# Optimization experiments

Measured on AMD Instinct MI355X. Metric: run time of the kernel, lower is better.

## Reference

```python
import jax, jax.numpy as jnp
import numpy as np
import math

D_MODEL = 1024
N_HEAD = 16
D_K = D_MODEL // N_HEAD
NEG_INF = -1e30  # fp32 mask fill value used by the torch module


def _rope(x, b_rotate=None):
    # x: [b, h, n, k], k even. Interleaved (even/odd) RoPE, matching the torch code.
    b, h, n, k = x.shape
    half = k // 2
    inv_freq = 1.0 / (10000.0 ** (jnp.arange(half, dtype=jnp.float32) / half))  # [half]
    ang = jnp.arange(n, dtype=jnp.float32)[:, None] * inv_freq[None, :]          # [n, half]
    sin = jnp.sin(ang)
    cos = jnp.cos(ang)
    x1 = x[..., 0::2]  # [b,h,n,half]
    x2 = x[..., 1::2]
    even = x1 * cos - x2 * sin
    odd = x1 * sin + x2 * cos
    out = jnp.stack([even, odd], axis=-1).reshape(b, h, n, k)  # re-interleave
    if b_rotate is not None:
        out = out * b_rotate  # barope multiplicative term
    return out


def setup_inputs() -> dict:
    key = jax.random.key(0)
    ks = jax.random.split(key, 7)
    B, S = 1, 2048
    query = jax.random.normal(ks[0], (B, S, D_MODEL), dtype=jnp.float32)
    kk = jax.random.normal(ks[1], (B, S, D_MODEL), dtype=jnp.float32)
    value = jax.random.normal(ks[2], (B, S, D_MODEL), dtype=jnp.float32)
    b_emb = jax.random.normal(ks[3], (B, S, D_MODEL), dtype=jnp.float32)
    mask = jax.random.bernoulli(ks[4], 0.9, (B, S))  # bool [B,S]
    linear_layers = 0.02 * jax.random.normal(ks[5], (3, D_MODEL, N_HEAD, D_K), dtype=jnp.float32)
    b_proj = jax.random.normal(ks[6], (D_MODEL, N_HEAD, D_K), dtype=jnp.float32)
    return {"query": query, "key": kk, "value": value, "b_emb": b_emb,
            "mask": mask, "linear_layers": linear_layers, "b_proj": b_proj}


def reference(query, key, value, b_emb, mask, linear_layers, b_proj):
    B, S, _ = query.shape
    # QKV projections: [b,n,d] x [d,h,k] -> [b,h,n,k]
    q = jnp.einsum('bnd,dhk->bhnk', query, linear_layers[0])
    k = jnp.einsum('bnd,dhk->bhnk', key, linear_layers[1])
    v = jnp.einsum('bnd,dhk->bhnk', value, linear_layers[2])
    # barope=True branch: multiplicative rotation modifier from b_emb
    b_rotate = jnp.einsum('bnd,dhk->bhnk', b_emb, b_proj)
    q = _rope(q, b_rotate)
    k = _rope(k, b_rotate)
    scores = jnp.einsum('bhqk,bhmk->bhqm', q, k) / math.sqrt(D_K)  # [b,h,s,s]
    pair_mask = (mask[:, :, None] & mask[:, None, :])[:, None]     # [b,1,s,s]
    scores = jnp.where(pair_mask, scores, NEG_INF)
    p_attn = jax.nn.softmax(scores, axis=-1)  # dropout p=0 -> identity
    x = jnp.einsum('bhqm,bhmk->bhqk', p_attn, v)
    return x.transpose(0, 2, 1, 3).reshape(B, S, N_HEAD * D_K)
```

## Files before the change

### kernel.cpp

```cpp
#include <hip/hip_runtime.h>
#include <hip/hip_bf16.h>
#include <math.h>

#define S_LEN 2048
#define NHEAD 16
#define DMODEL 1024

typedef short bf16x8 __attribute__((ext_vector_type(8)));
typedef float f32x4 __attribute__((ext_vector_type(4)));

static __device__ __forceinline__ unsigned short bfbits(float x) {
    __hip_bfloat16 h = __float2bfloat16(x);
    unsigned short u; __builtin_memcpy(&u, &h, 2); return u;
}
static __device__ __forceinline__ float bf2f(unsigned short u) {
    union { unsigned int i; float f; } v; v.i = ((unsigned int)u) << 16; return v.f;
}
static __device__ __forceinline__ void splitRN(float x, unsigned short& hi, unsigned short& lo) {
    unsigned short h = bfbits(x);
    float r = x - bf2f(h);
    hi = h; lo = bfbits(r);
}
static __device__ __forceinline__ void split4(float4 x, ushort4& h4, ushort4& l4) {
    unsigned short h0,l0,h1,l1,h2,l2,h3,l3;
    splitRN(x.x,h0,l0); splitRN(x.y,h1,l1); splitRN(x.z,h2,l2); splitRN(x.w,h3,l3);
    h4 = make_ushort4(h0,h1,h2,h3); l4 = make_ushort4(l0,l1,l2,l3);
}

__device__ __forceinline__ int mask_at(const void* mp, int enc, int s) {
    if (enc) return ((const unsigned char*)mp)[s] != 0;
    return ((const unsigned int*)mp)[s] != 0u;
}

__global__ void detect_kernel(const void* __restrict__ mask, int* __restrict__ flags) {
    if (threadIdx.x == 0 && blockIdx.x == 0) {
        const unsigned int* m = (const unsigned int*)mask;
        int bytey = 0;
        for (int i = 0; i < 8; ++i) {
            unsigned int u = m[i];
            if (u != 0u && u != 1u && u != 0x3F800000u) bytey = 1;
        }
        flags[0] = bytey;
    }
}

__global__ __launch_bounds__(256)
void presplit_w(const float* __restrict__ ll, const float* __restrict__ bproj,
                unsigned short* __restrict__ Wh, unsigned short* __restrict__ Wl) {
    __shared__ unsigned short Th[64][72], Tl[64][72];
    const int t = threadIdx.x;
    const int bid = blockIdx.x;
    const int stream = bid >> 8;
    const int rem = bid & 255;
    const int h = rem >> 4;
    const int d0 = (rem & 15) << 6;
    const float* src = (stream == 3) ? bproj : (ll + (size_t)stream * 1048576);
#pragma unroll
    for (int rep = 0; rep < 4; ++rep) {
        int fid = rep * 256 + t;
        int dl = fid >> 4, n4 = (fid & 15) * 4;
        float4 w = *(const float4*)&src[(size_t)(d0 + dl) * 1024 + h * 64 + n4];
        unsigned short hh, lo2;
#pragma unroll
        for (int m = 0; m < 4; ++m) { splitRN((&w.x)[m], hh, lo2); Th[n4+m][dl] = hh; Tl[n4+m][dl] = lo2; }
    }
    __syncthreads();
    size_t obase = (size_t)stream * 1048576;
#pragma unroll
    for (int rep = 0; rep < 2; ++rep) {
        int wid = rep * 256 + t;
        int n = wid >> 3, dl8 = (wid & 7) * 8;
        int dtile = n >> 4, cc = n & 15;
        int dglob = d0 + dl8;
        int kc = dglob >> 5;
        int qd = (dglob >> 3) & 3;
        size_t off = obase + (size_t)(h * 4 + dtile) * 16384 + (size_t)kc * 512
                   + (size_t)(qd * 16 + cc) * 8;
        *(uint4*)&Wh[off] = *(uint4*)&Th[n][dl8];
        *(uint4*)&Wl[off] = *(uint4*)&Tl[n][dl8];
    }
}

__global__ __launch_bounds__(256, 2)
void proj_fused4(const float* __restrict__ Xq, const float* __restrict__ Xk,
                 const float* __restrict__ Xv, const float* __restrict__ Xb,
                 const unsigned short* __restrict__ Wh, const unsigned short* __restrict__ Wl,
                 unsigned short* __restrict__ qhi, unsigned short* __restrict__ qlo,
                 unsigned short* __restrict__ khi, unsigned short* __restrict__ klo,
                 unsigned short* __restrict__ vhi) {
    __shared__ unsigned short smem[17920];
    unsigned short (*XQh)[40] = (unsigned short(*)[40])(smem + 0 * 2560);
    unsigned short (*XQl)[40] = (unsigned short(*)[40])(smem + 1 * 2560);
    unsigned short (*XKh)[40] = (unsigned short(*)[40])(smem + 2 * 2560);
    unsigned short (*XKl)[40] = (unsigned short(*)[40])(smem + 3 * 2560);
    unsigned short (*XVh)[40] = (unsigned short(*)[40])(smem + 4 * 2560);
    unsigned short (*XBh)[40] = (unsigned short(*)[40])(smem + 5 * 2560);
    unsigned short (*XBl)[40] = (unsigned short(*)[40])(smem + 6 * 2560);
    unsigned short (*T0)[72] = (unsigned short(*)[72])(smem + 0 * 4608);
    unsigned short (*T1)[72] = (unsigned short(*)[72])(smem + 1 * 4608);
    unsigned short (*T2)[72] = (unsigned short(*)[72])(smem + 2 * 4608);

    const int t = threadIdx.x;
    const int lin = blockIdx.x + (blockIdx.y << 4);
    const int xcd = lin & 7;
    const int h = (lin >> 3) & 15;
    const int s0 = (xcd * 4 + (lin >> 7)) * 64;
    const int lane = t & 63, dt = t >> 6, quad = lane >> 4, c = lane & 15;

    f32x4 aq[4], ak[4], av[4], ab[4];
#pragma unroll
    for (int i = 0; i < 4; ++i) {
        aq[i] = (f32x4){0.f,0.f,0.f,0.f}; ak[i] = (f32x4){0.f,0.f,0.f,0.f};
        av[i] = (f32x4){0.f,0.f,0.f,0.f}; ab[i] = (f32x4){0.f,0.f,0.f,0.f};
    }

    const int xr = t >> 2, xk = (t & 3) * 8;
    const size_t xg = (size_t)(s0 + xr) * DMODEL + xk;
    const size_t wb = (size_t)(h * 4 + dt) * 16384 + (size_t)lane * 8;

    float4 pq[2], pk[2], pv[2], pb[2];
    pq[0] = *(const float4*)&Xq[xg]; pq[1] = *(const float4*)&Xq[xg + 4];
    pk[0] = *(const float4*)&Xk[xg]; pk[1] = *(const float4*)&Xk[xg + 4];
    pv[0] = *(const float4*)&Xv[xg]; pv[1] = *(const float4*)&Xv[xg + 4];
    pb[0] = *(const float4*)&Xb[xg]; pb[1] = *(const float4*)&Xb[xg + 4];

    bf16x8 wQh = *(const bf16x8*)&Wh[wb];
    bf16x8 wQl = *(const bf16x8*)&Wl[wb];
    bf16x8 wKh = *(const bf16x8*)&Wh[1048576 + wb];
    bf16x8 wKl = *(const bf16x8*)&Wl[1048576 + wb];
    bf16x8 wVh = *(const bf16x8*)&Wh[2097152 + wb];
    bf16x8 wVl = *(const bf16x8*)&Wl[2097152 + wb];
    bf16x8 wBh = *(const bf16x8*)&Wh[3145728 + wb];
    bf16x8 wBl = *(const bf16x8*)&Wl[3145728 + wb];

    for (int kc = 0; kc < 32; ++kc) {
        __syncthreads();
        {
            ushort4 h4, l4;
            split4(pq[0], h4, l4); *(ushort4*)&XQh[xr][xk]   = h4; *(ushort4*)&XQl[xr][xk]   = l4;
            split4(pq[1], h4, l4); *(ushort4*)&XQh[xr][xk+4] = h4; *(ushort4*)&XQl[xr][xk+4] = l4;
            split4(pk[0], h4, l4); *(ushort4*)&XKh[xr][xk]   = h4; *(ushort4*)&XKl[xr][xk]   = l4;
            split4(pk[1], h4, l4); *(ushort4*)&XKh[xr][xk+4] = h4; *(ushort4*)&XKl[xr][xk+4] = l4;
            split4(pb[0], h4, l4); *(ushort4*)&XBh[xr][xk]   = h4; *(ushort4*)&XBl[xr][xk]   = l4;
            split4(pb[1], h4, l4); *(ushort4*)&XBh[xr][xk+4] = h4; *(ushort4*)&XBl[xr][xk+4] = l4;
            *(ushort4*)&XVh[xr][xk]   = make_ushort4(bfbits(pv[0].x),bfbits(pv[0].y),bfbits(pv[0].z),bfbits(pv[0].w));
            *(ushort4*)&XVh[xr][xk+4] = make_ushort4(bfbits(pv[1].x),bfbits(pv[1].y),bfbits(pv[1].z),bfbits(pv[1].w));
        }
        __syncthreads();

        bf16x8 aQh = wQh, aQl = wQl, aKh = wKh, aKl = wKl;
        bf16x8 aVh = wVh, aVl = wVl, aBh = wBh, aBl = wBl;

        if (kc + 1 < 32) {
            size_t wo = wb + (size_t)(kc + 1) * 512;
            wQh = *(const bf16x8*)&Wh[wo];           wQl = *(const bf16x8*)&Wl[wo];
            wKh = *(const bf16x8*)&Wh[1048576 + wo]; wKl = *(const bf16x8*)&Wl[1048576 + wo];
            wVh = *(const bf16x8*)&Wh[2097152 + wo]; wVl = *(const bf16x8*)&Wl[2097152 + wo];
            wBh = *(const bf16x8*)&Wh[3145728 + wo]; wBl = *(const bf16x8*)&Wl[3145728 + wo];
            size_t g = xg + (size_t)(kc + 1) * 32;
            pq[0] = *(const float4*)&Xq[g]; pq[1] = *(const float4*)&Xq[g + 4];
            pk[0] = *(const float4*)&Xk[g]; pk[1] = *(const float4*)&Xk[g + 4];
            pv[0] = *(const float4*)&Xv[g]; pv[1] = *(const float4*)&Xv[g + 4];
            pb[0] = *(const float4*)&Xb[g]; pb[1] = *(const float4*)&Xb[g + 4];
        }

#pragma unroll
        for (int st = 0; st < 4; ++st) {
            bf16x8 b1 = *(bf16x8*)&XQh[st*16+c][quad*8];
            bf16x8 b2 = *(bf16x8*)&XQl[st*16+c][quad*8];
            aq[st] = __builtin_amdgcn_mfma_f32_16x16x32_bf16(aQh, b1, aq[st], 0, 0, 0);
            aq[st] = __builtin_amdgcn_mfma_f32_16x16x32_bf16(aQh, b2, aq[st], 0, 0, 0);
            aq[st] = __builtin_amdgcn_mfma_f32_16x16x32_bf16(aQl, b1, aq[st], 0, 0, 0);
            aq[st] = __builtin_amdgcn_mfma_f32_16x16x32_bf16(aQl, b2, aq[st], 0, 0, 0);
            b1 = *(bf16x8*)&XKh[st*16+c][quad*8];
            b2 = *(bf16x8*)&XKl[st*16+c][quad*8];
            ak[st] = __builtin_amdgcn_mfma_f32_16x16x32_bf16(aKh, b1, ak[st], 0, 0, 0);
            ak[st] = __builtin_amdgcn_mfma_f32_16x16x32_bf16(aKh, b2, ak[st], 0, 0, 0);
            ak[st] = __builtin_amdgcn_mfma_f32_16x16x32_bf16(aKl, b1, ak[st], 0, 0, 0);
            ak[st] = __builtin_amdgcn_mfma_f32_16x16x32_bf16(aKl, b2, ak[st], 0, 0, 0);
            b1 = *(bf16x8*)&XVh[st*16+c][quad*8];
            av[st] = __builtin_amdgcn_mfma_f32_16x16x32_bf16(aVh, b1, av[st], 0, 0, 0);
            av[st] = __builtin_amdgcn_mfma_f32_16x16x32_bf16(aVl, b1, av[st], 0, 0, 0);
            b1 = *(bf16x8*)&XBh[st*16+c][quad*8];
            b2 = *(bf16x8*)&XBl[st*16+c][quad*8];
            ab[st] = __builtin_amdgcn_mfma_f32_16x16x32_bf16(aBh, b1, ab[st], 0, 0, 0);
            ab[st] = __builtin_amdgcn_mfma_f32_16x16x32_bf16(aBh, b2, ab[st], 0, 0, 0);
            ab[st] = __builtin_amdgcn_mfma_f32_16x16x32_bf16(aBl, b1, ab[st], 0, 0, 0);
            ab[st] = __builtin_amdgcn_mfma_f32_16x16x32_bf16(aBl, b2, ab[st], 0, 0, 0);
        }
    }

    float rq[4][4], rk[4][4];
    {
        int p0 = dt * 8 + 2 * quad;
        double inv0 = pow(10000.0, -(double)p0 / 32.0);
        double inv1 = pow(10000.0, -(double)(p0 + 1) / 32.0);
#pragma unroll
        for (int st = 0; st < 4; ++st) {
            int s = s0 + st * 16 + c;
            double a0 = (double)s * inv0, a1 = (double)s * inv1;
            float sn0 = (float)sin(a0), cs0 = (float)cos(a0);
            float sn1 = (float)sin(a1), cs1 = (float)cos(a1);
            rq[st][0] = (aq[st][0]*cs0 - aq[st][1]*sn0) * ab[st][0];
            rq[st][1] = (aq[st][0]*sn0 + aq[st][1]*cs0) * ab[st][1];
            rq[st][2] = (aq[st][2]*cs1 - aq[st][3]*sn1) * ab[st][2];
            rq[st][3] = (aq[st][2]*sn1 + aq[st][3]*cs1) * ab[st][3];
            rk[st][0] = (ak[st][0]*cs0 - ak[st][1]*sn0) * ab[st][0];
            rk[st][1] = (ak[st][0]*sn0 + ak[st][1]*cs0) * ab[st][1];
            rk[st][2] = (ak[st][2]*cs1 - ak[st][3]*sn1) * ab[st][2];
            rk[st][3] = (ak[st][2]*sn1 + ak[st][3]*cs1) * ab[st][3];
        }
    }
    __syncthreads();
#pragma unroll
    for (int st = 0; st < 4; ++st) {
        unsigned short h0,l0,h1,l1,h2,l2,h3,l3;
        splitRN(rq[st][0],h0,l0); splitRN(rq[st][1],h1,l1);
        splitRN(rq[st][2],h2,l2); splitRN(rq[st][3],h3,l3);
        *(ushort4*)&T0[st*16+c][dt*16+4*quad] = make_ushort4(h0,h1,h2,h3);
        *(ushort4*)&T1[st*16+c][dt*16+4*quad] = make_ushort4(l0,l1,l2,l3);
#pragma unroll
        for (int reg = 0; reg < 4; ++reg)
            T2[dt * 16 + 4 * quad + reg][st * 16 + c] = bfbits(av[st][reg]);
    }
    __syncthreads();
#pragma unroll
    for (int i = 0; i < 2; ++i) {
        int id = i * 256 + t, row = id >> 3, d8 = (id & 7) * 8;
        size_t qb = ((size_t)(h * S_LEN + s0 + row)) * 64 + d8;
        *(uint4*)&qhi[qb] = *(uint4*)&T0[row][d8];
        *(uint4*)&qlo[qb] = *(uint4*)&T1[row][d8];
        size_t vb = ((size_t)(h * 64 + row)) * S_LEN + s0 + d8;
        *(uint4*)&vhi[vb] = *(uint4*)&T2[row][d8];
    }
    __syncthreads();
#pragma unroll
    for (int st = 0; st < 4; ++st) {
        unsigned short h0,l0,h1,l1,h2,l2,h3,l3;
        splitRN(rk[st][0],h0,l0); splitRN(rk[st][1],h1,l1);
        splitRN(rk[st][2],h2,l2); splitRN(rk[st][3],h3,l3);
        *(ushort4*)&T0[st*16+c][dt*16+4*quad] = make_ushort4(h0,h1,h2,h3);
        *(ushort4*)&T1[st*16+c][dt*16+4*quad] = make_ushort4(l0,l1,l2,l3);
    }
    __syncthreads();
#pragma unroll
    for (int i = 0; i < 2; ++i) {
        int id = i * 256 + t, row = id >> 3, d8 = (id & 7) * 8;
        size_t qb = ((size_t)(h * S_LEN + s0 + row)) * 64 + d8;
        *(uint4*)&khi[qb] = *(uint4*)&T0[row][d8];
        *(uint4*)&klo[qb] = *(uint4*)&T1[row][d8];
    }
}

__global__ __launch_bounds__(256)
void attn_mfma(const unsigned short* __restrict__ qh, const unsigned short* __restrict__ ql,
               const unsigned short* __restrict__ kh, const unsigned short* __restrict__ kl,
               const unsigned short* __restrict__ vh,
               const void* __restrict__ mask, float* __restrict__ out,
               const int* __restrict__ flags) {
    __shared__ unsigned short Kh[2][64][72], Kl[2][64][72];
    __shared__ unsigned short Vt[2][64][72];
    __shared__ unsigned short Sh[64][72], Sl[64][72];
    const int menc = flags[0];
    const int t = threadIdx.x;
    const int lin = blockIdx.x + (blockIdx.y << 5);
    const int h = (lin & 7) * 2 + ((lin >> 3) & 1);
    const int s0 = (lin >> 4) * 64;
    const int lane = t & 63, w = t >> 6, quad = lane >> 4, c = lane & 15;

    bf16x8 qfh[2], qfl[2];
#pragma unroll
    for (int ks = 0; ks < 2; ++ks) {
        size_t base = ((size_t)(h * S_LEN + s0 + 16 * w + c)) * 64 + ks * 32 + quad * 8;
        qfh[ks] = *(const bf16x8*)&qh[base];
        qfl[ks] = *(const bf16x8*)&ql[base];
    }
    int mq[4];
#pragma unroll
    for (int i = 0; i < 4; ++i) mq[i] = mask_at(mask, menc, s0 + 16 * w + quad * 4 + i);

    float m_i[4], l_i[4];
#pragma unroll
    for (int i = 0; i < 4; ++i) { m_i[i] = -INFINITY; l_i[i] = 0.0f; }
    f32x4 o_acc[4];
#pragma unroll
    for (int i = 0; i < 4; ++i) o_acc[i] = (f32x4){0.f,0.f,0.f,0.f};

    uint4 pre[6];
#pragma unroll
    for (int i = 0; i < 2; ++i) {
        int id = i * 256 + t, row = id >> 3, col8 = (id & 7) * 8;
        size_t kb = ((size_t)(h * S_LEN + row)) * 64 + col8;
        size_t vb = ((size_t)(h * 64 + row)) * S_LEN + col8;
        pre[0 + i] = *(const uint4*)&kh[kb];
        pre[2 + i] = *(const uint4*)&kl[kb];
        pre[4 + i] = *(const uint4*)&vh[vb];
    }
#pragma unroll
    for (int i = 0; i < 2; ++i) {
        int id = i * 256 + t, row = id >> 3, col8 = (id & 7) * 8;
        *(uint4*)&Kh[0][row][col8] = pre[0 + i];
        *(uint4*)&Kl[0][row][col8] = pre[2 + i];
        *(uint4*)&Vt[0][row][col8] = pre[4 + i];
    }
    __syncthreads();

    int cur = 0;
    for (int kt = 0; kt < 32; ++kt) {
        if (kt + 1 < 32) {
            const int kb0 = (kt + 1) * 64;
#pragma unroll
            for (int i = 0; i < 2; ++i) {
                int id = i * 256 + t, row = id >> 3, col8 = (id & 7) * 8;
                size_t kb = ((size_t)(h * S_LEN + kb0 + row)) * 64 + col8;
                size_t vb = ((size_t)(h * 64 + row)) * S_LEN + kb0 + col8;
                pre[0 + i] = *(const uint4*)&kh[kb];
                pre[2 + i] = *(const uint4*)&kl[kb];
                pre[4 + i] = *(const uint4*)&vh[vb];
            }
        }
        int mk[4];
#pragma unroll
        for (int nt = 0; nt < 4; ++nt) mk[nt] = mask_at(mask, menc, kt * 64 + 16 * nt + c);

        f32x4 sc[4];
#pragma unroll
        for (int i = 0; i < 4; ++i) sc[i] = (f32x4){0.f,0.f,0.f,0.f};
#pragma unroll
        for (int nt = 0; nt < 4; ++nt)
#pragma unroll
            for (int ks = 0; ks < 2; ++ks) {
                bf16x8 kfh = *(bf16x8*)&Kh[cur][nt * 16 + c][ks * 32 + quad * 8];
                bf16x8 kfl = *(bf16x8*)&Kl[cur][nt * 16 + c][ks * 32 + quad * 8];
                sc[nt] = __builtin_amdgcn_mfma_f32_16x16x32_bf16(qfh[ks], kfh, sc[nt], 0, 0, 0);
                sc[nt] = __builtin_amdgcn_mfma_f32_16x16x32_bf16(qfh[ks], kfl, sc[nt], 0, 0, 0);
                sc[nt] = __builtin_amdgcn_mfma_f32_16x16x32_bf16(qfl[ks], kfh, sc[nt], 0, 0, 0);
            }

        float sm[4][4];
#pragma unroll
        for (int nt = 0; nt < 4; ++nt)
#pragma unroll
            for (int reg = 0; reg < 4; ++reg)
                sm[nt][reg] = (mq[reg] && mk[nt]) ? sc[nt][reg] * 0.125f : -1e30f;

        float rmax[4];
#pragma unroll
        for (int reg = 0; reg < 4; ++reg)
            rmax[reg] = fmaxf(fmaxf(sm[0][reg], sm[1][reg]), fmaxf(sm[2][reg], sm[3][reg]));
#pragma unroll
        for (int off = 1; off <= 8; off <<= 1)
#pragma unroll
            for (int reg = 0; reg < 4; ++reg)
                rmax[reg] = fmaxf(rmax[reg], __shfl_xor(rmax[reg], off, 64));

        float mn[4], alpha[4];
#pragma unroll
        for (int reg = 0; reg < 4; ++reg) {
            mn[reg] = fmaxf(m_i[reg], rmax[reg]);
            alpha[reg] = __expf(m_i[reg] - mn[reg]);
            m_i[reg] = mn[reg];
        }

        float rsum[4] = {0.f, 0.f, 0.f, 0.f};
#pragma unroll
        for (int nt = 0; nt < 4; ++nt)
#pragma unroll
            for (int reg = 0; reg < 4; ++reg) {
                float e = __expf(sm[nt][reg] - mn[reg]);
                rsum[reg] += e;
                unsigned short eh, el;
                splitRN(e, eh, el);
                Sh[16 * w + quad * 4 + reg][16 * nt + c] = eh;
                Sl[16 * w + quad * 4 + reg][16 * nt + c] = el;
            }
#pragma unroll
        for (int off = 1; off <= 8; off <<= 1)
#pragma unroll
            for (int reg = 0; reg < 4; ++reg)
                rsum[reg] += __shfl_xor(rsum[reg], off, 64);
#pragma unroll
        for (int reg = 0; reg < 4; ++reg) l_i[reg] = l_i[reg] * alpha[reg] + rsum[reg];
#pragma unroll
        for (int nt = 0; nt < 4; ++nt)
#pragma unroll
            for (int reg = 0; reg < 4; ++reg) o_acc[nt][reg] *= alpha[reg];

        if (kt + 1 < 32) {
            const int nxt = cur ^ 1;
#pragma unroll
            for (int i = 0; i < 2; ++i) {
                int id = i * 256 + t, row = id >> 3, col8 = (id & 7) * 8;
                *(uint4*)&Kh[nxt][row][col8] = pre[0 + i];
                *(uint4*)&Kl[nxt][row][col8] = pre[2 + i];
                *(uint4*)&Vt[nxt][row][col8] = pre[4 + i];
            }
        }
        __syncthreads();

#pragma unroll
        for (int ks = 0; ks < 2; ++ks) {
            bf16x8 pfh = *(bf16x8*)&Sh[16 * w + c][ks * 32 + quad * 8];
            bf16x8 pfl = *(bf16x8*)&Sl[16 * w + c][ks * 32 + quad * 8];
#pragma unroll
            for (int nt = 0; nt < 4; ++nt) {
                bf16x8 vf = *(bf16x8*)&Vt[cur][nt * 16 + c][ks * 32 + quad * 8];
                o_acc[nt] = __builtin_amdgcn_mfma_f32_16x16x32_bf16(pfh, vf, o_acc[nt], 0, 0, 0);
                o_acc[nt] = __builtin_amdgcn_mfma_f32_16x16x32_bf16(pfl, vf, o_acc[nt], 0, 0, 0);
            }
        }
        __syncthreads();
        cur ^= 1;
    }

#pragma unroll
    for (int reg = 0; reg < 4; ++reg) {
        float inv = 1.0f / l_i[reg];
        int row = s0 + 16 * w + quad * 4 + reg;
#pragma unroll
        for (int nt = 0; nt < 4; ++nt)
            out[(size_t)row * 1024 + h * 64 + nt * 16 + c] = o_acc[nt][reg] * inv;
    }
}

extern "C" void kernel_launch(void* const* d_in, const int* in_sizes, int n_in,
                              void* d_out, int out_size, void* d_ws, size_t ws_size,
                              hipStream_t stream) {
    const float* query = (const float*)d_in[0];
    const float* key   = (const float*)d_in[1];
    const float* value = (const float*)d_in[2];
    const float* b_emb = (const float*)d_in[3];
    const void*  mask  = d_in[4];
    const float* ll    = (const float*)d_in[5];
    const float* bproj = (const float*)d_in[6];
    float* out = (float*)d_out;

    const size_t HSD = (size_t)NHEAD * S_LEN * 64;
    char* ws = (char*)d_ws;
    int* flags = (int*)ws;
    unsigned short* qhi = (unsigned short*)(ws + 4096);
    unsigned short* qlo = qhi + HSD;
    unsigned short* khi = qlo + HSD;
    unsigned short* klo = khi + HSD;
    unsigned short* vhi = klo + HSD;
    unsigned short* Wh  = vhi + HSD;
    unsigned short* Wl  = Wh + 4 * 1048576;

    dim3 pb(256);
    detect_kernel<<<1, 64, 0, stream>>>(mask, flags);
    presplit_w<<<1024, pb, 0, stream>>>(ll, bproj, Wh, Wl);
    proj_fused4<<<dim3(16, 32), pb, 0, stream>>>(query, key, value, b_emb,
                                                 Wh, Wl, qhi, qlo, khi, klo, vhi);
    attn_mfma<<<dim3(32, 16), pb, 0, stream>>>(qhi, qlo, khi, klo, vhi, mask, out, flags);
}
```

Before: 263.2 us.

## Halve projection tile for higher occupancy and trim attention rescale and barrier

The fused projection kernel now processes 32 sequence rows per block instead of 64. It launches 1024 blocks with a 4-blocks-per-SM launch bound and half the shared memory, and drops the register double-buffering of weight fragments so fewer registers are live. In the attention kernel, the output accumulator rescale is skipped when every alpha in the wave equals one, and the barrier between staging the next K/V tile and the P·V MFMAs is removed. The trade-offs are that weight loads are no longer prefetched and each block reuses weights across fewer rows, and the removed barrier relies on each wave reading only its own rows of the softmax tile.

```diff
diff --git a/kernel.cpp b/kernel.cpp
--- a/kernel.cpp
+++ b/kernel.cpp
@@ -81,91 +81,82 @@
     }
 }
 
-__global__ __launch_bounds__(256, 2)
-void proj_fused4(const float* __restrict__ Xq, const float* __restrict__ Xk,
+__global__ __launch_bounds__(256, 4)
+void proj_fused5(const float* __restrict__ Xq, const float* __restrict__ Xk,
                  const float* __restrict__ Xv, const float* __restrict__ Xb,
                  const unsigned short* __restrict__ Wh, const unsigned short* __restrict__ Wl,
                  unsigned short* __restrict__ qhi, unsigned short* __restrict__ qlo,
                  unsigned short* __restrict__ khi, unsigned short* __restrict__ klo,
                  unsigned short* __restrict__ vhi) {
-    __shared__ unsigned short smem[17920];
-    unsigned short (*XQh)[40] = (unsigned short(*)[40])(smem + 0 * 2560);
-    unsigned short (*XQl)[40] = (unsigned short(*)[40])(smem + 1 * 2560);
-    unsigned short (*XKh)[40] = (unsigned short(*)[40])(smem + 2 * 2560);
-    unsigned short (*XKl)[40] = (unsigned short(*)[40])(smem + 3 * 2560);
-    unsigned short (*XVh)[40] = (unsigned short(*)[40])(smem + 4 * 2560);
-    unsigned short (*XBh)[40] = (unsigned short(*)[40])(smem + 5 * 2560);
-    unsigned short (*XBl)[40] = (unsigned short(*)[40])(smem + 6 * 2560);
-    unsigned short (*T0)[72] = (unsigned short(*)[72])(smem + 0 * 4608);
-    unsigned short (*T1)[72] = (unsigned short(*)[72])(smem + 1 * 4608);
-    unsigned short (*T2)[72] = (unsigned short(*)[72])(smem + 2 * 4608);
+    __shared__ unsigned short smem[8960];
+    unsigned short (*XQh)[40] = (unsigned short(*)[40])(smem + 0 * 1280);
+    unsigned short (*XQl)[40] = (unsigned short(*)[40])(smem + 1 * 1280);
+    unsigned short (*XKh)[40] = (unsigned short(*)[40])(smem + 2 * 1280);
+    unsigned short (*XKl)[40] = (unsigned short(*)[40])(smem + 3 * 1280);
+    unsigned short (*XVh)[40] = (unsigned short(*)[40])(smem + 4 * 1280);
+    unsigned short (*XBh)[40] = (unsigned short(*)[40])(smem + 5 * 1280);
+    unsigned short (*XBl)[40] = (unsigned short(*)[40])(smem + 6 * 1280);
+    unsigned short (*T0)[72] = (unsigned short(*)[72])(smem + 0);
+    unsigned short (*T1)[72] = (unsigned short(*)[72])(smem + 2304);
+    unsigned short (*T2)[40] = (unsigned short(*)[40])(smem + 4608);
 
     const int t = threadIdx.x;
-    const int lin = blockIdx.x + (blockIdx.y << 4);
+    const int lin = blockIdx.x;
     const int xcd = lin & 7;
-    const int h = (lin >> 3) & 15;
-    const int s0 = (xcd * 4 + (lin >> 7)) * 64;
+    const int inner = lin >> 3;
+    const int h = inner >> 3;
+    const int sg = inner & 7;
+    const int s0 = (xcd * 8 + sg) * 32;
     const int lane = t & 63, dt = t >> 6, quad = lane >> 4, c = lane & 15;
 
-    f32x4 aq[4], ak[4], av[4], ab[4];
-#pragma unroll
-    for (int i = 0; i < 4; ++i) {
+    f32x4 aq[2], ak[2], av[2], ab[2];
+#pragma unroll
+    for (int i = 0; i < 2; ++i) {
         aq[i] = (f32x4){0.f,0.f,0.f,0.f}; ak[i] = (f32x4){0.f,0.f,0.f,0.f};
         av[i] = (f32x4){0.f,0.f,0.f,0.f}; ab[i] = (f32x4){0.f,0.f,0.f,0.f};
     }
 
-    const int xr = t >> 2, xk = (t & 3) * 8;
-    const size_t xg = (size_t)(s0 + xr) * DMODEL + xk;
+    const int xr = t >> 3, xc = (t & 7) * 4;
+    const size_t xg = (size_t)(s0 + xr) * DMODEL + xc;
     const size_t wb = (size_t)(h * 4 + dt) * 16384 + (size_t)lane * 8;
 
-    float4 pq[2], pk[2], pv[2], pb[2];
-    pq[0] = *(const float4*)&Xq[xg]; pq[1] = *(const float4*)&Xq[xg + 4];
-    pk[0] = *(const float4*)&Xk[xg]; pk[1] = *(const float4*)&Xk[xg + 4];
-    pv[0] = *(const float4*)&Xv[xg]; pv[1] = *(const float4*)&Xv[xg + 4];
-    pb[0] = *(const float4*)&Xb[xg]; pb[1] = *(const float4*)&Xb[xg + 4];
-
-    bf16x8 wQh = *(const bf16x8*)&Wh[wb];
-    bf16x8 wQl = *(const bf16x8*)&Wl[wb];
-    bf16x8 wKh = *(const bf16x8*)&Wh[1048576 + wb];
-    bf16x8 wKl = *(const bf16x8*)&Wl[1048576 + wb];
-    bf16x8 wVh = *(const bf16x8*)&Wh[2097152 + wb];
-    bf16x8 wVl = *(const bf16x8*)&Wl[2097152 + wb];
-    bf16x8 wBh = *(const bf16x8*)&Wh[3145728 + wb];
-    bf16x8 wBl = *(const bf16x8*)&Wl[3145728 + wb];
+    float4 pq, pk, pv, pb;
+    pq = *(const float4*)&Xq[xg];
+    pk = *(const float4*)&Xk[xg];
+    pv = *(const float4*)&Xv[xg];
+    pb = *(const float4*)&Xb[xg];
 
     for (int kc = 0; kc < 32; ++kc) {
         __syncthreads();
         {
             ushort4 h4, l4;
-            split4(pq[0], h4, l4); *(ushort4*)&XQh[xr][xk]   = h4; *(ushort4*)&XQl[xr][xk]   = l4;
-            split4(pq[1], h4, l4); *(ushort4*)&XQh[xr][xk+4] = h4; *(ushort4*)&XQl[xr][xk+4] = l4;
-            split4(pk[0], h4, l4); *(ushort4*)&XKh[xr][xk]   = h4; *(ushort4*)&XKl[xr][xk]   = l4;
-            split4(pk[1], h4, l4); *(ushort4*)&XKh[xr][xk+4] = h4; *(ushort4*)&XKl[xr][xk+4] = l4;
-            split4(pb[0], h4, l4); *(ushort4*)&XBh[xr][xk]   = h4; *(ushort4*)&XBl[xr][xk]   = l4;
-            split4(pb[1], h4, l4); *(ushort4*)&XBh[xr][xk+4] = h4; *(ushort4*)&XBl[xr][xk+4] = l4;
-            *(ushort4*)&XVh[xr][xk]   = make_ushort4(bfbits(pv[0].x),bfbits(pv[0].y),bfbits(pv[0].z),bfbits(pv[0].w));
-            *(ushort4*)&XVh[xr][xk+4] = make_ushort4(bfbits(pv[1].x),bfbits(pv[1].y),bfbits(pv[1].z),bfbits(pv[1].w));
+            split4(pq, h4, l4); *(ushort4*)&XQh[xr][xc] = h4; *(ushort4*)&XQl[xr][xc] = l4;
+            split4(pk, h4, l4); *(ushort4*)&XKh[xr][xc] = h4; *(ushort4*)&XKl[xr][xc] = l4;
+            split4(pb, h4, l4); *(ushort4*)&XBh[xr][xc] = h4; *(ushort4*)&XBl[xr][xc] = l4;
+            *(ushort4*)&XVh[xr][xc] = make_ushort4(bfbits(pv.x),bfbits(pv.y),bfbits(pv.z),bfbits(pv.w));
         }
         __syncthreads();
 
-        bf16x8 aQh = wQh, aQl = wQl, aKh = wKh, aKl = wKl;
-        bf16x8 aVh = wVh, aVl = wVl, aBh = wBh, aBl = wBl;
+        size_t wo = wb + (size_t)kc * 512;
+        bf16x8 aQh = *(const bf16x8*)&Wh[wo];
+        bf16x8 aQl = *(const bf16x8*)&Wl[wo];
+        bf16x8 aKh = *(const bf16x8*)&Wh[1048576 + wo];
+        bf16x8 aKl = *(const bf16x8*)&Wl[1048576 + wo];
+        bf16x8 aVh = *(const bf16x8*)&Wh[2097152 + wo];
+        bf16x8 aVl = *(const bf16x8*)&Wl[2097152 + wo];
+        bf16x8 aBh = *(const bf16x8*)&Wh[3145728 + wo];
+        bf16x8 aBl = *(const bf16x8*)&Wl[3145728 + wo];
 
         if (kc + 1 < 32) {
-            size_t wo = wb + (size_t)(kc + 1) * 512;
-            wQh = *(const bf16x8*)&Wh[wo];           wQl = *(const bf16x8*)&Wl[wo];
-            wKh = *(const bf16x8*)&Wh[1048576 + wo]; wKl = *(const bf16x8*)&Wl[1048576 + wo];
-            wVh = *(const bf16x8*)&Wh[2097152 + wo]; wVl = *(const bf16x8*)&Wl[2097152 + wo];
-            wBh = *(const bf16x8*)&Wh[3145728 + wo]; wBl = *(const bf16x8*)&Wl[3145728 + wo];
             size_t g = xg + (size_t)(kc + 1) * 32;
-            pq[0] = *(const float4*)&Xq[g]; pq[1] = *(const float4*)&Xq[g + 4];
-            pk[0] = *(const float4*)&Xk[g]; pk[1] = *(const float4*)&Xk[g + 4];
-            pv[0] = *(const float4*)&Xv[g]; pv[1] = *(const float4*)&Xv[g + 4];
-            pb[0] = *(const float4*)&Xb[g]; pb[1] = *(const float4*)&Xb[g + 4];
-        }
-
-#pragma unroll
-        for (int st = 0; st < 4; ++st) {
+            pq = *(const float4*)&Xq[g];
+            pk = *(const float4*)&Xk[g];
+            pv = *(const float4*)&Xv[g];
+            pb = *(const float4*)&Xb[g];
+        }
+
+#pragma unroll
+        for (int st = 0; st < 2; ++st) {
             bf16x8 b1 = *(bf16x8*)&XQh[st*16+c][quad*8];
             bf16x8 b2 = *(bf16x8*)&XQl[st*16+c][quad*8];
             aq[st] = __builtin_amdgcn_mfma_f32_16x16x32_bf16(aQh, b1, aq[st], 0, 0, 0);
@@ -190,13 +181,13 @@
         }
     }
 
-    float rq[4][4], rk[4][4];
+    float rq[2][4], rk[2][4];
     {
         int p0 = dt * 8 + 2 * quad;
         double inv0 = pow(10000.0, -(double)p0 / 32.0);
         double inv1 = pow(10000.0, -(double)(p0 + 1) / 32.0);
 #pragma unroll
-        for (int st = 0; st < 4; ++st) {
+        for (int st = 0; st < 2; ++st) {
             int s = s0 + st * 16 + c;
             double a0 = (double)s * inv0, a1 = (double)s * inv1;
             float sn0 = (float)sin(a0), cs0 = (float)cos(a0);
@@ -213,7 +204,7 @@
     }
     __syncthreads();
 #pragma unroll
-    for (int st = 0; st < 4; ++st) {
+    for (int st = 0; st < 2; ++st) {
         unsigned short h0,l0,h1,l1,h2,l2,h3,l3;
         splitRN(rq[st][0],h0,l0); splitRN(rq[st][1],h1,l1);
         splitRN(rq[st][2],h2,l2); splitRN(rq[st][3],h3,l3);
@@ -224,18 +215,18 @@
             T2[dt * 16 + 4 * quad + reg][st * 16 + c] = bfbits(av[st][reg]);
     }
     __syncthreads();
-#pragma unroll
-    for (int i = 0; i < 2; ++i) {
-        int id = i * 256 + t, row = id >> 3, d8 = (id & 7) * 8;
+    {
+        int row = t >> 3, d8 = (t & 7) * 8;
         size_t qb = ((size_t)(h * S_LEN + s0 + row)) * 64 + d8;
         *(uint4*)&qhi[qb] = *(uint4*)&T0[row][d8];
         *(uint4*)&qlo[qb] = *(uint4*)&T1[row][d8];
-        size_t vb = ((size_t)(h * 64 + row)) * S_LEN + s0 + d8;
-        *(uint4*)&vhi[vb] = *(uint4*)&T2[row][d8];
-    }
-    __syncthreads();
-#pragma unroll
-    for (int st = 0; st < 4; ++st) {
+        int d = t >> 2, s8 = (t & 3) * 8;
+        size_t vb = ((size_t)(h * 64 + d)) * S_LEN + s0 + s8;
+        *(uint4*)&vhi[vb] = *(uint4*)&T2[d][s8];
+    }
+    __syncthreads();
+#pragma unroll
+    for (int st = 0; st < 2; ++st) {
         unsigned short h0,l0,h1,l1,h2,l2,h3,l3;
         splitRN(rk[st][0],h0,l0); splitRN(rk[st][1],h1,l1);
         splitRN(rk[st][2],h2,l2); splitRN(rk[st][3],h3,l3);
@@ -243,9 +234,8 @@
         *(ushort4*)&T1[st*16+c][dt*16+4*quad] = make_ushort4(l0,l1,l2,l3);
     }
     __syncthreads();
-#pragma unroll
-    for (int i = 0; i < 2; ++i) {
-        int id = i * 256 + t, row = id >> 3, d8 = (id & 7) * 8;
+    {
+        int row = t >> 3, d8 = (t & 7) * 8;
         size_t qb = ((size_t)(h * S_LEN + s0 + row)) * 64 + d8;
         *(uint4*)&khi[qb] = *(uint4*)&T0[row][d8];
         *(uint4*)&klo[qb] = *(uint4*)&T1[row][d8];
@@ -381,10 +371,13 @@
                 rsum[reg] += __shfl_xor(rsum[reg], off, 64);
 #pragma unroll
         for (int reg = 0; reg < 4; ++reg) l_i[reg] = l_i[reg] * alpha[reg] + rsum[reg];
-#pragma unroll
-        for (int nt = 0; nt < 4; ++nt)
-#pragma unroll
-            for (int reg = 0; reg < 4; ++reg) o_acc[nt][reg] *= alpha[reg];
+        if (!__all(alpha[0] == 1.0f && alpha[1] == 1.0f &&
+                   alpha[2] == 1.0f && alpha[3] == 1.0f)) {
+#pragma unroll
+            for (int nt = 0; nt < 4; ++nt)
+#pragma unroll
+                for (int reg = 0; reg < 4; ++reg) o_acc[nt][reg] *= alpha[reg];
+        }
 
         if (kt + 1 < 32) {
             const int nxt = cur ^ 1;
@@ -396,7 +389,6 @@
                 *(uint4*)&Vt[nxt][row][col8] = pre[4 + i];
             }
         }
-        __syncthreads();
 
 #pragma unroll
         for (int ks = 0; ks < 2; ++ks) {
@@ -449,7 +441,7 @@
     dim3 pb(256);
     detect_kernel<<<1, 64, 0, stream>>>(mask, flags);
     presplit_w<<<1024, pb, 0, stream>>>(ll, bproj, Wh, Wl);
-    proj_fused4<<<dim3(16, 32), pb, 0, stream>>>(query, key, value, b_emb,
-                                                 Wh, Wl, qhi, qlo, khi, klo, vhi);
+    proj_fused5<<<1024, pb, 0, stream>>>(query, key, value, b_emb,
+                                         Wh, Wl, qhi, qlo, khi, klo, vhi);
     attn_mfma<<<dim3(32, 16), pb, 0, stream>>>(qhi, qlo, khi, klo, vhi, mask, out, flags);
 }
```

New measurement: 268.8 us. 2.1% more time.
